# Kernel optimization log

Hardware: AMD Instinct MI355X
Metric: run time of the kernel (lower is better)

Reference implementation:

```python
import jax, jax.numpy as jnp
import numpy as np

B, D_IN, D_OUT, E = 8192, 1024, 1024, 16


def setup_inputs() -> dict:
    key = jax.random.key(0)
    k1, k2, k3 = jax.random.split(key, 3)
    x = jax.random.normal(k1, (B, D_IN), dtype=jnp.float32)
    Wg = jax.random.normal(k2, (D_IN, E), dtype=jnp.float32) * (1.0 / np.sqrt(D_IN))
    bg = jnp.zeros((E,), dtype=jnp.float32)
    We = jax.random.normal(k3, (E, D_IN, D_OUT), dtype=jnp.float32) * (1.0 / np.sqrt(D_IN))
    be = jnp.zeros((E, D_OUT), dtype=jnp.float32)
    return {"x": x, "Wg": Wg, "bg": bg, "We": We, "be": be}


def reference(x, Wg, bg, We, be):
    # Gate: [B, E]
    gate_out = x @ Wg + bg
    top1 = jnp.argmax(gate_out, axis=1)  # [B]
    # All-expert dense compute (faithful to the naive HardMoE): [B, E, D_OUT]
    expert_outs = jnp.einsum('bd,edh->beh', x, We) + be[None, :, :]
    # Gather each row's argmax expert output: [B, D_OUT]
    out = jnp.take_along_axis(expert_outs, top1[:, None, None], axis=1)[:, 0, :]
    return out
```

## Files before the change

### kernel.cpp

```cpp
#include <hip/hip_runtime.h>

typedef unsigned short u16;
typedef __attribute__((ext_vector_type(4))) unsigned short u16x4;
typedef __attribute__((ext_vector_type(8))) short short8;
typedef __attribute__((ext_vector_type(4))) float floatx4;

#define NB 8192
#define DK 1024
#define DN 1024
#define NE 16
#define TM 128
#define TN 128
#define BK 64
#define MAX_TILES 80
#define GTHR 4e-3f

__device__ __forceinline__ u16 f2bf(float f) {
    union { float f; unsigned int u; } v; v.f = f;
    unsigned int u = v.u;
    return (u16)((u + 0x7fffu + ((u >> 16) & 1u)) >> 16);
}

__device__ __forceinline__ float bf2f(u16 h) {
    union { unsigned int u; float f; } v; v.u = ((unsigned int)h) << 16;
    return v.f;
}

__device__ __forceinline__ void gld16(const void* g, void* l) {
    __builtin_amdgcn_global_load_lds(
        (const __attribute__((address_space(1))) unsigned int*)g,
        (__attribute__((address_space(3))) unsigned int*)l, 16, 0, 0);
}

__global__ __launch_bounds__(256) void k_gate(const float* __restrict__ x,
                                              const float* __restrict__ Wg,
                                              const float* __restrict__ bg,
                                              u16* __restrict__ xb,
                                              int* __restrict__ cnt,
                                              int* __restrict__ bucket,
                                              int* __restrict__ fixcnt,
                                              int* __restrict__ fixlist) {
    __shared__ u16 xsh[4][16 * 64];
    __shared__ u16 xsl[4][16 * 64];
    __shared__ u16 wgh[4][16 * 64];
    __shared__ u16 wgl[4][16 * 64];
    __shared__ float gred[4][16 * 17];

    const int tid = threadIdx.x;
    const int lane = tid & 63;
    const int w = tid >> 6;
    const int lr = lane & 15, q = lane >> 4;
    const int R0 = blockIdx.x * 16;
    const int kw = w * 256;

    floatx4 acc = (floatx4)0.0f;

    for (int cc = 0; cc < 4; ++cc) {
        const int kc = kw + cc * 64;
        #pragma unroll
        for (int i = 0; i < 2; ++i) {
            int c = i * 64 + lane;
            int r = c >> 3, s8 = c & 7;
            const float* gp = &x[(size_t)(R0 + r) * DK + kc + s8 * 8];
            float4 v0 = *(const float4*)gp;
            float4 v1 = *(const float4*)(gp + 4);
            float vv[8] = { v0.x, v0.y, v0.z, v0.w, v1.x, v1.y, v1.z, v1.w };
            u16 hi[8], lo[8];
            #pragma unroll
            for (int j = 0; j < 8; ++j) {
                hi[j] = f2bf(vv[j]);
                lo[j] = f2bf(vv[j] - bf2f(hi[j]));
            }
            int a = r * 64 + ((s8 ^ (r & 7)) * 8);
            *(short8*)&xsh[w][a] = *(const short8*)hi;
            *(short8*)&xsl[w][a] = *(const short8*)lo;
            *(short8*)&xb[(size_t)(R0 + r) * DK + kc + s8 * 8] = *(const short8*)hi;
        }
        #pragma unroll
        for (int i = 0; i < 4; ++i) {
            int f = i * 64 + lane;
            int k = f >> 2;
            int e4 = (f & 3) * 4;
            float4 v = *(const float4*)&Wg[(size_t)(kc + k) * NE + e4];
            int s = k >> 3, j = k & 7;
            float vv[4] = { v.x, v.y, v.z, v.w };
            #pragma unroll
            for (int t = 0; t < 4; ++t) {
                int er = e4 + t;
                u16 hi = f2bf(vv[t]);
                u16 lo = f2bf(vv[t] - bf2f(hi));
                int a = er * 64 + ((s ^ (er & 7)) * 8 + j);
                wgh[w][a] = hi;
                wgl[w][a] = lo;
            }
        }
        __syncthreads();
        #pragma unroll
        for (int kwin = 0; kwin < 2; ++kwin) {
            int sg = kwin * 4 + q;
            int ab = lr * 64 + ((sg ^ (lr & 7)) * 8);
            short8 bh = *(const short8*)&wgh[w][ab];
            short8 bl = *(const short8*)&wgl[w][ab];
            short8 ah = *(const short8*)&xsh[w][ab];
            short8 al = *(const short8*)&xsl[w][ab];
            acc = __builtin_amdgcn_mfma_f32_16x16x32_bf16(ah, bh, acc, 0, 0, 0);
            acc = __builtin_amdgcn_mfma_f32_16x16x32_bf16(ah, bl, acc, 0, 0, 0);
            acc = __builtin_amdgcn_mfma_f32_16x16x32_bf16(al, bh, acc, 0, 0, 0);
        }
        __syncthreads();
    }

    #pragma unroll
    for (int rr = 0; rr < 4; ++rr)
        gred[w][(q * 4 + rr) * 17 + lr] = acc[rr];
    __syncthreads();

    if (tid < 16) {
        int row = R0 + tid;
        float g[16];
        #pragma unroll
        for (int e = 0; e < 16; ++e)
            g[e] = gred[0][tid * 17 + e] + gred[1][tid * 17 + e]
                 + gred[2][tid * 17 + e] + gred[3][tid * 17 + e] + bg[e];
        float best = g[0], second = -1e30f; int bi = 0;
        #pragma unroll
        for (int e = 1; e < 16; ++e) {
            if (g[e] > best) { second = best; best = g[e]; bi = e; }
            else if (g[e] > second) second = g[e];
        }
        if (best - second >= GTHR) {
            int pos = atomicAdd(&cnt[bi], 1);
            bucket[bi * NB + pos] = row;
        } else {
            int f = atomicAdd(fixcnt, 1);
            fixlist[f] = row;
        }
    }
}

__global__ __launch_bounds__(256) void k_fix(const float* __restrict__ x,
                                             const float* __restrict__ Wg,
                                             const float* __restrict__ bg,
                                             const int* __restrict__ fixcnt,
                                             const int* __restrict__ fixlist,
                                             int* __restrict__ cnt,
                                             int* __restrict__ bucket) {
    __shared__ double lred[4][16];
    const int tid = threadIdx.x;
    const int lane = tid & 63;
    const int w = tid >> 6;
    const int n = *fixcnt;
    for (int it = blockIdx.x; it < n; it += 256) {
        const int row = fixlist[it];
        float4 xv = *(const float4*)&x[(size_t)row * DK + tid * 4];
        const float* xf = (const float*)&xv;
        double acc[16];
        #pragma unroll
        for (int e = 0; e < 16; ++e) acc[e] = 0.0;
        #pragma unroll
        for (int j = 0; j < 4; ++j) {
            int k = tid * 4 + j;
            double xd = (double)xf[j];
            const float4* wr = (const float4*)&Wg[(size_t)k * NE];
            float4 w0 = wr[0], w1 = wr[1], w2 = wr[2], w3 = wr[3];
            acc[0]  += xd * (double)w0.x;  acc[1]  += xd * (double)w0.y;
            acc[2]  += xd * (double)w0.z;  acc[3]  += xd * (double)w0.w;
            acc[4]  += xd * (double)w1.x;  acc[5]  += xd * (double)w1.y;
            acc[6]  += xd * (double)w1.z;  acc[7]  += xd * (double)w1.w;
            acc[8]  += xd * (double)w2.x;  acc[9]  += xd * (double)w2.y;
            acc[10] += xd * (double)w2.z;  acc[11] += xd * (double)w2.w;
            acc[12] += xd * (double)w3.x;  acc[13] += xd * (double)w3.y;
            acc[14] += xd * (double)w3.z;  acc[15] += xd * (double)w3.w;
        }
        #pragma unroll
        for (int e = 0; e < 16; ++e) {
            double v = acc[e];
            #pragma unroll
            for (int off = 1; off < 64; off <<= 1)
                v += __shfl_xor(v, off);
            acc[e] = v;
        }
        if (lane == 0) {
            #pragma unroll
            for (int e = 0; e < 16; ++e) lred[w][e] = acc[e];
        }
        __syncthreads();
        if (tid == 0) {
            double best = -1e300; int bi = 0;
            #pragma unroll
            for (int e = 0; e < 16; ++e) {
                double g = lred[0][e] + lred[1][e] + lred[2][e] + lred[3][e]
                         + (double)bg[e];
                if (g > best) { best = g; bi = e; }
            }
            int pos = atomicAdd(&cnt[bi], 1);
            bucket[bi * NB + pos] = row;
        }
        __syncthreads();
    }
}

__global__ __launch_bounds__(256) void k_wet(const float* __restrict__ We,
                                             u16* __restrict__ WeT) {
    __shared__ float t[64 * 65];
    const int bw = blockIdx.x;
    const int e  = bw >> 8;
    const int n0 = ((bw >> 4) & 15) * 64;
    const int k0 = (bw & 15) * 64;
    const int tid = threadIdx.x;
    const float* src = We + (size_t)e * DK * DN;

    const int n4 = (tid & 15) * 4;
    const int kl = tid >> 4;
    #pragma unroll
    for (int r = 0; r < 4; ++r) {
        int k = r * 16 + kl;
        float4 v = *(const float4*)&src[(size_t)(k0 + k) * DN + n0 + n4];
        t[k * 65 + n4 + 0] = v.x;
        t[k * 65 + n4 + 1] = v.y;
        t[k * 65 + n4 + 2] = v.z;
        t[k * 65 + n4 + 3] = v.w;
    }
    __syncthreads();
    u16* dst = WeT + (size_t)e * DN * DK;
    #pragma unroll
    for (int r = 0; r < 2; ++r) {
        int idx = r * 256 + tid;
        int nl = idx >> 3;
        int k8 = idx & 7;
        u16 pk[8];
        #pragma unroll
        for (int i = 0; i < 8; ++i)
            pk[i] = f2bf(t[(k8 * 8 + i) * 65 + nl]);
        *(short8*)&dst[(size_t)(n0 + nl) * DK + k0 + k8 * 8] = *(const short8*)pk;
    }
}

__global__ __launch_bounds__(256) void k_moe(const u16* __restrict__ xb,
                                             const u16* __restrict__ WeT,
                                             const float* __restrict__ be,
                                             const int* __restrict__ bucket,
                                             const int* __restrict__ cnt,
                                             float* __restrict__ out) {
    const int slot = blockIdx.x >> 3;
    const int nt = blockIdx.x & 7;

    int e = -1, mt = 0, cntE = 0, acc_t = 0;
    #pragma unroll
    for (int ee = 0; ee < NE; ++ee) {
        int ce = cnt[ee];
        int nte = (ce + TM - 1) / TM;
        if (e < 0 && slot < acc_t + nte) { e = ee; mt = slot - acc_t; cntE = ce; }
        acc_t += nte;
    }
    if (e < 0) return;

    const int m0 = mt * TM;
    const int n0 = nt * TN;

    __shared__ u16 aLds[TM * BK];
    __shared__ u16 bLds[TN * BK];

    const int tid = threadIdx.x;
    const int lane = tid & 63;
    const int w = tid >> 6;
    const int wr = w >> 1, wc = w & 1;
    const int lr = lane & 15, q = lane >> 4;

    long aoff[4]; long boff[4]; int ldsb[4];
    #pragma unroll
    for (int r = 0; r < 4; ++r) {
        int c = r * 256 + tid;
        int row = c >> 3;
        int k8 = (c & 7) ^ (row & 7);
        int m_idx = m0 + row; if (m_idx >= cntE) m_idx = cntE - 1;
        long rid = bucket[e * NB + m_idx];
        aoff[r] = rid * DK + k8 * 8;
        boff[r] = (long)e * DN * DK + (long)(n0 + row) * DK + k8 * 8;
        ldsb[r] = (r * 256 + (tid & ~63)) * 8;
    }

    floatx4 acc[4][4];
    #pragma unroll
    for (int mi = 0; mi < 4; ++mi)
        #pragma unroll
        for (int ni = 0; ni < 4; ++ni)
            acc[mi][ni] = (floatx4)0.0f;

    for (int kk = 0; kk < DK; kk += BK) {
        #pragma unroll
        for (int r = 0; r < 4; ++r) {
            gld16(xb + aoff[r] + kk, &aLds[ldsb[r]]);
            gld16(WeT + boff[r] + kk, &bLds[ldsb[r]]);
        }
        __syncthreads();
        #pragma unroll
        for (int ks = 0; ks < 2; ++ks) {
            short8 af[4], bfr[4];
            const int slot_k = ((ks << 2) + q) ^ (lr & 7);
            #pragma unroll
            for (int mi = 0; mi < 4; ++mi) {
                int row = wr * 64 + mi * 16 + lr;
                af[mi] = *(const short8*)&aLds[row * BK + slot_k * 8];
                int nrow = wc * 64 + mi * 16 + lr;
                bfr[mi] = *(const short8*)&bLds[nrow * BK + slot_k * 8];
            }
            #pragma unroll
            for (int mi = 0; mi < 4; ++mi)
                #pragma unroll
                for (int ni = 0; ni < 4; ++ni)
                    acc[mi][ni] = __builtin_amdgcn_mfma_f32_16x16x32_bf16(
                        af[mi], bfr[ni], acc[mi][ni], 0, 0, 0);
        }
        __syncthreads();
    }

    float bias[4];
    #pragma unroll
    for (int ni = 0; ni < 4; ++ni)
        bias[ni] = be[e * DN + n0 + wc * 64 + ni * 16 + lr];

    #pragma unroll
    for (int mi = 0; mi < 4; ++mi) {
        #pragma unroll
        for (int rr = 0; rr < 4; ++rr) {
            int row_l = wr * 64 + mi * 16 + q * 4 + rr;
            int m_idx = m0 + row_l;
            if (m_idx < cntE) {
                long rid = bucket[e * NB + m_idx];
                float* orow = out + rid * DN + n0 + wc * 64 + lr;
                #pragma unroll
                for (int ni = 0; ni < 4; ++ni)
                    orow[ni * 16] = acc[mi][ni][rr] + bias[ni];
            }
        }
    }
}

extern "C" void kernel_launch(void* const* d_in, const int* in_sizes, int n_in,
                              void* d_out, int out_size, void* d_ws, size_t ws_size,
                              hipStream_t stream) {
    const float* x  = (const float*)d_in[0];
    const float* Wg = (const float*)d_in[1];
    const float* bg = (const float*)d_in[2];
    const float* We = (const float*)d_in[3];
    const float* be = (const float*)d_in[4];
    float* out = (float*)d_out;

    int* cnt     = (int*)d_ws;
    int* fixcnt  = cnt + 16;
    int* fixlist = cnt + 32;
    int* bucket  = cnt + 8448;
    u16* xb  = (u16*)((char*)d_ws + (1u << 20));
    u16* wet = (u16*)((char*)d_ws + (18u << 20));

    hipMemsetAsync(cnt, 0, 20 * sizeof(int), stream);
    k_gate<<<512, 256, 0, stream>>>(x, Wg, bg, xb, cnt, bucket, fixcnt, fixlist);
    k_fix<<<256, 256, 0, stream>>>(x, Wg, bg, fixcnt, fixlist, cnt, bucket);
    k_wet<<<4096, 256, 0, stream>>>(We, wet);
    k_moe<<<MAX_TILES * 8, 256, 0, stream>>>(xb, wet, be, bucket, cnt, out);
}
```

Measured before the change: 232.7 us.

## Merge gate and weight-transpose kernels; double GEMM K-tile to 128

The gate kernel and the expert-weight transpose/bf16 conversion kernel become one launch, with blocks split by index and shared memory overlaid through a union. This removes a kernel launch and lets the gate and transpose work run concurrently on the GPU. Separately, the expert GEMM K tile grows from 64 to 128 with a 16-way XOR swizzle, halving the number of barrier-separated iterations. The cost is doubled LDS use per block (64KB), which may lower occupancy.

Result: faster. 216.7 us (-6.9%).

```diff
diff --git a/kernel.cpp b/kernel.cpp
--- a/kernel.cpp
+++ b/kernel.cpp
@@ -11,9 +11,12 @@
 #define NE 16
 #define TM 128
 #define TN 128
-#define BK 64
+#define BK 128
 #define MAX_TILES 80
 #define GTHR 4e-3f
+
+#define GATE_BLOCKS 512
+#define WET_BLOCKS  4096
 
 __device__ __forceinline__ u16 f2bf(float f) {
     union { float f; unsigned int u; } v; v.f = f;
@@ -32,108 +35,150 @@
         (__attribute__((address_space(3))) unsigned int*)l, 16, 0, 0);
 }
 
-__global__ __launch_bounds__(256) void k_gate(const float* __restrict__ x,
+__global__ __launch_bounds__(256) void k_prep(const float* __restrict__ x,
                                               const float* __restrict__ Wg,
                                               const float* __restrict__ bg,
+                                              const float* __restrict__ We,
                                               u16* __restrict__ xb,
+                                              u16* __restrict__ WeT,
                                               int* __restrict__ cnt,
                                               int* __restrict__ bucket,
                                               int* __restrict__ fixcnt,
                                               int* __restrict__ fixlist) {
-    __shared__ u16 xsh[4][16 * 64];
-    __shared__ u16 xsl[4][16 * 64];
-    __shared__ u16 wgh[4][16 * 64];
-    __shared__ u16 wgl[4][16 * 64];
-    __shared__ float gred[4][16 * 17];
+    __shared__ union {
+        struct {
+            u16 xsh[4][16 * 64];
+            u16 xsl[4][16 * 64];
+            u16 wgh[4][16 * 64];
+            u16 wgl[4][16 * 64];
+            float gred[4][16 * 17];
+        } g;
+        float t[64 * 65];
+    } sh;
 
     const int tid = threadIdx.x;
-    const int lane = tid & 63;
-    const int w = tid >> 6;
-    const int lr = lane & 15, q = lane >> 4;
-    const int R0 = blockIdx.x * 16;
-    const int kw = w * 256;
-
-    floatx4 acc = (floatx4)0.0f;
-
-    for (int cc = 0; cc < 4; ++cc) {
-        const int kc = kw + cc * 64;
-        #pragma unroll
-        for (int i = 0; i < 2; ++i) {
-            int c = i * 64 + lane;
-            int r = c >> 3, s8 = c & 7;
-            const float* gp = &x[(size_t)(R0 + r) * DK + kc + s8 * 8];
-            float4 v0 = *(const float4*)gp;
-            float4 v1 = *(const float4*)(gp + 4);
-            float vv[8] = { v0.x, v0.y, v0.z, v0.w, v1.x, v1.y, v1.z, v1.w };
-            u16 hi[8], lo[8];
-            #pragma unroll
-            for (int j = 0; j < 8; ++j) {
-                hi[j] = f2bf(vv[j]);
-                lo[j] = f2bf(vv[j] - bf2f(hi[j]));
-            }
-            int a = r * 64 + ((s8 ^ (r & 7)) * 8);
-            *(short8*)&xsh[w][a] = *(const short8*)hi;
-            *(short8*)&xsl[w][a] = *(const short8*)lo;
-            *(short8*)&xb[(size_t)(R0 + r) * DK + kc + s8 * 8] = *(const short8*)hi;
-        }
-        #pragma unroll
-        for (int i = 0; i < 4; ++i) {
-            int f = i * 64 + lane;
-            int k = f >> 2;
-            int e4 = (f & 3) * 4;
-            float4 v = *(const float4*)&Wg[(size_t)(kc + k) * NE + e4];
-            int s = k >> 3, j = k & 7;
-            float vv[4] = { v.x, v.y, v.z, v.w };
-            #pragma unroll
-            for (int t = 0; t < 4; ++t) {
-                int er = e4 + t;
-                u16 hi = f2bf(vv[t]);
-                u16 lo = f2bf(vv[t] - bf2f(hi));
-                int a = er * 64 + ((s ^ (er & 7)) * 8 + j);
-                wgh[w][a] = hi;
-                wgl[w][a] = lo;
-            }
-        }
-        __syncthreads();
-        #pragma unroll
-        for (int kwin = 0; kwin < 2; ++kwin) {
-            int sg = kwin * 4 + q;
-            int ab = lr * 64 + ((sg ^ (lr & 7)) * 8);
-            short8 bh = *(const short8*)&wgh[w][ab];
-            short8 bl = *(const short8*)&wgl[w][ab];
-            short8 ah = *(const short8*)&xsh[w][ab];
-            short8 al = *(const short8*)&xsl[w][ab];
-            acc = __builtin_amdgcn_mfma_f32_16x16x32_bf16(ah, bh, acc, 0, 0, 0);
-            acc = __builtin_amdgcn_mfma_f32_16x16x32_bf16(ah, bl, acc, 0, 0, 0);
-            acc = __builtin_amdgcn_mfma_f32_16x16x32_bf16(al, bh, acc, 0, 0, 0);
-        }
-        __syncthreads();
-    }
-
-    #pragma unroll
-    for (int rr = 0; rr < 4; ++rr)
-        gred[w][(q * 4 + rr) * 17 + lr] = acc[rr];
-    __syncthreads();
-
-    if (tid < 16) {
-        int row = R0 + tid;
-        float g[16];
-        #pragma unroll
-        for (int e = 0; e < 16; ++e)
-            g[e] = gred[0][tid * 17 + e] + gred[1][tid * 17 + e]
-                 + gred[2][tid * 17 + e] + gred[3][tid * 17 + e] + bg[e];
-        float best = g[0], second = -1e30f; int bi = 0;
-        #pragma unroll
-        for (int e = 1; e < 16; ++e) {
-            if (g[e] > best) { second = best; best = g[e]; bi = e; }
-            else if (g[e] > second) second = g[e];
-        }
-        if (best - second >= GTHR) {
-            int pos = atomicAdd(&cnt[bi], 1);
-            bucket[bi * NB + pos] = row;
-        } else {
-            int f = atomicAdd(fixcnt, 1);
-            fixlist[f] = row;
+
+    if (blockIdx.x < GATE_BLOCKS) {
+        const int lane = tid & 63;
+        const int w = tid >> 6;
+        const int lr = lane & 15, q = lane >> 4;
+        const int R0 = blockIdx.x * 16;
+        const int kw = w * 256;
+
+        floatx4 acc = (floatx4)0.0f;
+
+        for (int cc = 0; cc < 4; ++cc) {
+            const int kc = kw + cc * 64;
+            #pragma unroll
+            for (int i = 0; i < 2; ++i) {
+                int c = i * 64 + lane;
+                int r = c >> 3, s8 = c & 7;
+                const float* gp = &x[(size_t)(R0 + r) * DK + kc + s8 * 8];
+                float4 v0 = *(const float4*)gp;
+                float4 v1 = *(const float4*)(gp + 4);
+                float vv[8] = { v0.x, v0.y, v0.z, v0.w, v1.x, v1.y, v1.z, v1.w };
+                u16 hi[8], lo[8];
+                #pragma unroll
+                for (int j = 0; j < 8; ++j) {
+                    hi[j] = f2bf(vv[j]);
+                    lo[j] = f2bf(vv[j] - bf2f(hi[j]));
+                }
+                int a = r * 64 + ((s8 ^ (r & 7)) * 8);
+                *(short8*)&sh.g.xsh[w][a] = *(const short8*)hi;
+                *(short8*)&sh.g.xsl[w][a] = *(const short8*)lo;
+                *(short8*)&xb[(size_t)(R0 + r) * DK + kc + s8 * 8] = *(const short8*)hi;
+            }
+            #pragma unroll
+            for (int i = 0; i < 4; ++i) {
+                int f = i * 64 + lane;
+                int k = f >> 2;
+                int e4 = (f & 3) * 4;
+                float4 v = *(const float4*)&Wg[(size_t)(kc + k) * NE + e4];
+                int s = k >> 3, j = k & 7;
+                float vv[4] = { v.x, v.y, v.z, v.w };
+                #pragma unroll
+                for (int t2 = 0; t2 < 4; ++t2) {
+                    int er = e4 + t2;
+                    u16 hi = f2bf(vv[t2]);
+                    u16 lo = f2bf(vv[t2] - bf2f(hi));
+                    int a = er * 64 + ((s ^ (er & 7)) * 8 + j);
+                    sh.g.wgh[w][a] = hi;
+                    sh.g.wgl[w][a] = lo;
+                }
+            }
+            __syncthreads();
+            #pragma unroll
+            for (int kwin = 0; kwin < 2; ++kwin) {
+                int sg = kwin * 4 + q;
+                int ab = lr * 64 + ((sg ^ (lr & 7)) * 8);
+                short8 bh = *(const short8*)&sh.g.wgh[w][ab];
+                short8 bl = *(const short8*)&sh.g.wgl[w][ab];
+                short8 ah = *(const short8*)&sh.g.xsh[w][ab];
+                short8 al = *(const short8*)&sh.g.xsl[w][ab];
+                acc = __builtin_amdgcn_mfma_f32_16x16x32_bf16(ah, bh, acc, 0, 0, 0);
+                acc = __builtin_amdgcn_mfma_f32_16x16x32_bf16(ah, bl, acc, 0, 0, 0);
+                acc = __builtin_amdgcn_mfma_f32_16x16x32_bf16(al, bh, acc, 0, 0, 0);
+            }
+            __syncthreads();
+        }
+
+        #pragma unroll
+        for (int rr = 0; rr < 4; ++rr)
+            sh.g.gred[w][(q * 4 + rr) * 17 + lr] = acc[rr];
+        __syncthreads();
+
+        if (tid < 16) {
+            int row = R0 + tid;
+            float g[16];
+            #pragma unroll
+            for (int e = 0; e < 16; ++e)
+                g[e] = sh.g.gred[0][tid * 17 + e] + sh.g.gred[1][tid * 17 + e]
+                     + sh.g.gred[2][tid * 17 + e] + sh.g.gred[3][tid * 17 + e] + bg[e];
+            float best = g[0], second = -1e30f; int bi = 0;
+            #pragma unroll
+            for (int e = 1; e < 16; ++e) {
+                if (g[e] > best) { second = best; best = g[e]; bi = e; }
+                else if (g[e] > second) second = g[e];
+            }
+            if (best - second >= GTHR) {
+                int pos = atomicAdd(&cnt[bi], 1);
+                bucket[bi * NB + pos] = row;
+            } else {
+                int f = atomicAdd(fixcnt, 1);
+                fixlist[f] = row;
+            }
+        }
+    } else {
+        const int bw = blockIdx.x - GATE_BLOCKS;
+        const int e  = bw >> 8;
+        const int n0 = ((bw >> 4) & 15) * 64;
+        const int k0 = (bw & 15) * 64;
+        const float* src = We + (size_t)e * DK * DN;
+        float* t = sh.t;
+
+        const int n4 = (tid & 15) * 4;
+        const int kl = tid >> 4;
+        #pragma unroll
+        for (int r = 0; r < 4; ++r) {
+            int k = r * 16 + kl;
+            float4 v = *(const float4*)&src[(size_t)(k0 + k) * DN + n0 + n4];
+            t[k * 65 + n4 + 0] = v.x;
+            t[k * 65 + n4 + 1] = v.y;
+            t[k * 65 + n4 + 2] = v.z;
+            t[k * 65 + n4 + 3] = v.w;
+        }
+        __syncthreads();
+        u16* dst = WeT + (size_t)e * DN * DK;
+        #pragma unroll
+        for (int r = 0; r < 2; ++r) {
+            int idx = r * 256 + tid;
+            int nl = idx >> 3;
+            int k8 = idx & 7;
+            u16 pk[8];
+            #pragma unroll
+            for (int i = 0; i < 8; ++i)
+                pk[i] = f2bf(t[(k8 * 8 + i) * 65 + nl]);
+            *(short8*)&dst[(size_t)(n0 + nl) * DK + k0 + k8 * 8] = *(const short8*)pk;
         }
     }
 }
@@ -200,42 +245,6 @@
     }
 }
 
-__global__ __launch_bounds__(256) void k_wet(const float* __restrict__ We,
-                                             u16* __restrict__ WeT) {
-    __shared__ float t[64 * 65];
-    const int bw = blockIdx.x;
-    const int e  = bw >> 8;
-    const int n0 = ((bw >> 4) & 15) * 64;
-    const int k0 = (bw & 15) * 64;
-    const int tid = threadIdx.x;
-    const float* src = We + (size_t)e * DK * DN;
-
-    const int n4 = (tid & 15) * 4;
-    const int kl = tid >> 4;
-    #pragma unroll
-    for (int r = 0; r < 4; ++r) {
-        int k = r * 16 + kl;
-        float4 v = *(const float4*)&src[(size_t)(k0 + k) * DN + n0 + n4];
-        t[k * 65 + n4 + 0] = v.x;
-        t[k * 65 + n4 + 1] = v.y;
-        t[k * 65 + n4 + 2] = v.z;
-        t[k * 65 + n4 + 3] = v.w;
-    }
-    __syncthreads();
-    u16* dst = WeT + (size_t)e * DN * DK;
-    #pragma unroll
-    for (int r = 0; r < 2; ++r) {
-        int idx = r * 256 + tid;
-        int nl = idx >> 3;
-        int k8 = idx & 7;
-        u16 pk[8];
-        #pragma unroll
-        for (int i = 0; i < 8; ++i)
-            pk[i] = f2bf(t[(k8 * 8 + i) * 65 + nl]);
-        *(short8*)&dst[(size_t)(n0 + nl) * DK + k0 + k8 * 8] = *(const short8*)pk;
-    }
-}
-
 __global__ __launch_bounds__(256) void k_moe(const u16* __restrict__ xb,
                                              const u16* __restrict__ WeT,
                                              const float* __restrict__ be,
@@ -267,16 +276,16 @@
     const int wr = w >> 1, wc = w & 1;
     const int lr = lane & 15, q = lane >> 4;
 
-    long aoff[4]; long boff[4]; int ldsb[4];
-    #pragma unroll
-    for (int r = 0; r < 4; ++r) {
+    long aoff[8]; long boff[8]; int ldsb[8];
+    #pragma unroll
+    for (int r = 0; r < 8; ++r) {
         int c = r * 256 + tid;
-        int row = c >> 3;
-        int k8 = (c & 7) ^ (row & 7);
+        int row = c >> 4;
+        int k16 = (c & 15) ^ (row & 15);
         int m_idx = m0 + row; if (m_idx >= cntE) m_idx = cntE - 1;
         long rid = bucket[e * NB + m_idx];
-        aoff[r] = rid * DK + k8 * 8;
-        boff[r] = (long)e * DN * DK + (long)(n0 + row) * DK + k8 * 8;
+        aoff[r] = rid * DK + k16 * 8;
+        boff[r] = (long)e * DN * DK + (long)(n0 + row) * DK + k16 * 8;
         ldsb[r] = (r * 256 + (tid & ~63)) * 8;
     }
 
@@ -289,21 +298,22 @@
 
     for (int kk = 0; kk < DK; kk += BK) {
         #pragma unroll
-        for (int r = 0; r < 4; ++r) {
+        for (int r = 0; r < 8; ++r)
             gld16(xb + aoff[r] + kk, &aLds[ldsb[r]]);
+        #pragma unroll
+        for (int r = 0; r < 8; ++r)
             gld16(WeT + boff[r] + kk, &bLds[ldsb[r]]);
-        }
-        __syncthreads();
-        #pragma unroll
-        for (int ks = 0; ks < 2; ++ks) {
+        __syncthreads();
+        #pragma unroll
+        for (int ks = 0; ks < 4; ++ks) {
+            const int kt = ks * 4 + q;
             short8 af[4], bfr[4];
-            const int slot_k = ((ks << 2) + q) ^ (lr & 7);
             #pragma unroll
             for (int mi = 0; mi < 4; ++mi) {
                 int row = wr * 64 + mi * 16 + lr;
-                af[mi] = *(const short8*)&aLds[row * BK + slot_k * 8];
+                af[mi] = *(const short8*)&aLds[row * BK + ((kt ^ (row & 15)) * 8)];
                 int nrow = wc * 64 + mi * 16 + lr;
-                bfr[mi] = *(const short8*)&bLds[nrow * BK + slot_k * 8];
+                bfr[mi] = *(const short8*)&bLds[nrow * BK + ((kt ^ (nrow & 15)) * 8)];
             }
             #pragma unroll
             for (int mi = 0; mi < 4; ++mi)
@@ -355,8 +365,8 @@
     u16* wet = (u16*)((char*)d_ws + (18u << 20));
 
     hipMemsetAsync(cnt, 0, 20 * sizeof(int), stream);
-    k_gate<<<512, 256, 0, stream>>>(x, Wg, bg, xb, cnt, bucket, fixcnt, fixlist);
+    k_prep<<<GATE_BLOCKS + WET_BLOCKS, 256, 0, stream>>>(x, Wg, bg, We, xb, wet,
+                                                         cnt, bucket, fixcnt, fixlist);
     k_fix<<<256, 256, 0, stream>>>(x, Wg, bg, fixcnt, fixlist, cnt, bucket);
-    k_wet<<<4096, 256, 0, stream>>>(We, wet);
     k_moe<<<MAX_TILES * 8, 256, 0, stream>>>(xb, wet, be, bucket, cnt, out);
 }
```
